# Kernel tuning notes

Hardware: AMD Instinct MI355X
Metric: run time of the kernel (lower is better)

The kernel has to match this reference:

```python
import jax, jax.numpy as jnp
import numpy as np
import math

HID = 1024
NH = 16
DH = HID // NH
B, S = 2, 2048

def _rel_shift(x):
    # x: [i, j, b, n] -> Transformer-XL relative shift
    i, j, b, n = x.shape
    xp = jnp.pad(x, ((0, 0), (1, 0), (0, 0), (0, 0)))  # [i, j+1, b, n]
    xp = xp.reshape(j + 1, i, b, n)
    return xp[1:].reshape(i, j, b, n)

def setup_inputs() -> dict:
    key = jax.random.key(0)
    ks = jax.random.split(key, 10)
    sc = 1.0 / math.sqrt(HID)
    return {
        "hidden_states": jax.random.normal(ks[0], (B, S, HID), jnp.float32),
        "r": jax.random.normal(ks[1], (S, HID), jnp.float32),
        "r_w_bias": jax.random.normal(ks[2], (NH, DH), jnp.float32) * 0.02,
        "r_r_bias": jax.random.normal(ks[3], (NH, DH), jnp.float32) * 0.02,
        "Wq": jax.random.normal(ks[4], (HID, HID), jnp.float32) * sc,
        "bq": jnp.zeros((HID,), jnp.float32),
        "Wk": jax.random.normal(ks[5], (HID, HID), jnp.float32) * sc,
        "bk": jnp.zeros((HID,), jnp.float32),
        "Wv": jax.random.normal(ks[6], (HID, HID), jnp.float32) * sc,
        "bv": jnp.zeros((HID,), jnp.float32),
        "Wr": jax.random.normal(ks[7], (HID, HID), jnp.float32) * sc,
    }

def reference(hidden_states, r, r_w_bias, r_r_bias, Wq, bq, Wk, bk, Wv, bv, Wr):
    b, s, h = hidden_states.shape
    # projections (weights stored [in, out])
    q = (hidden_states @ Wq + bq).reshape(b, s, NH, DH).transpose(1, 0, 2, 3)  # [s,b,nh,d]
    k = (hidden_states @ Wk + bk).reshape(b, s, NH, DH).transpose(1, 0, 2, 3)  # [s,b,nh,d]
    v = (hidden_states @ Wv + bv).reshape(b, s, NH, DH).transpose(0, 2, 1, 3)  # [b,nh,s,d]
    r_head_k = (r @ Wr).reshape(s, NH, DH)  # [rlen,nh,d]
    # content (AC) and position (BD) terms
    AC = jnp.einsum('ibnd,jbnd->ijbn', q + r_w_bias, k)
    BD = _rel_shift(jnp.einsum('ibnd,jnd->ijbn', q + r_r_bias, r_head_k))
    scores = (AC + BD).transpose(2, 3, 0, 1) / math.sqrt(DH)  # [b,nh,q,k]
    probs = jax.nn.softmax(scores, axis=-1)
    ctx = jnp.matmul(probs, v)  # [b,nh,q,d]
    ctx = ctx.transpose(0, 2, 1, 3).reshape(b, s, h)
    return ctx
```

## Files before the change

### kernel.cpp

```cpp
#include <hip/hip_runtime.h>
#include <math.h>

#define HID   1024
#define NHEAD 16
#define DHEAD 64
#define BATCH 2
#define SEQ   2048

#define TQ   64
#define TK2  128
#define NW2  191
#define LDP  136
#define LDBT 68

#define KSPLIT 2048
#define HEADSZ ((size_t)BATCH * SEQ * HID)

typedef __bf16 bf16_t;
typedef bf16_t bf16x8 __attribute__((ext_vector_type(8)));
typedef bf16_t bf16x4 __attribute__((ext_vector_type(4)));
typedef float  f32x4  __attribute__((ext_vector_type(4)));

__device__ __forceinline__ void load_lds16(const void* g, void* l) {
    __builtin_amdgcn_global_load_lds(
        (const __attribute__((address_space(1))) unsigned int*)g,
        (__attribute__((address_space(3))) unsigned int*)l, 16, 0, 0);
}

__device__ __forceinline__ void wg_barrier() {
    asm volatile("s_waitcnt lgkmcnt(0)" ::: "memory");
    __builtin_amdgcn_s_barrier();
    asm volatile("" ::: "memory");
}

__device__ __forceinline__ void split2(float x, bf16_t* hi, bf16_t* lo) {
    bf16_t h = (bf16_t)x;
    *hi = h;
    *lo = (bf16_t)(x - (float)h);
}

__global__ __launch_bounds__(256) void split_interleave(
    const float* __restrict__ in, bf16_t* __restrict__ out, int n4)
{
    int g = blockIdx.x * 256 + threadIdx.x;
    if (g >= n4) return;
    float4 v = ((const float4*)in)[g];
    int m = g >> 8, c4 = g & 255;
    float xs[4] = {v.x, v.y, v.z, v.w};
    bf16x8 o;
#pragma unroll
    for (int e = 0; e < 4; e++) {
        bf16_t h, l; split2(xs[e], &h, &l);
        o[2 * e] = h; o[2 * e + 1] = l;
    }
    *(bf16x8*)(out + (size_t)m * KSPLIT + c4 * 8) = o;
}

__global__ __launch_bounds__(256) void transpose_split3(
    const float* __restrict__ W0, const float* __restrict__ W1,
    const float* __restrict__ W2, bf16_t* __restrict__ WtBase)
{
    __shared__ float t[64][65];
    const int z = blockIdx.z;
    const float* W = (z == 0) ? W0 : (z == 1) ? W1 : W2;
    bf16_t* Wt = WtBase + (size_t)z * 1024 * KSPLIT;
    const int tid = threadIdx.x;
    const int n0 = blockIdx.x * 64, k0 = blockIdx.y * 64;
    for (int idx = tid; idx < 1024; idx += 256) {
        int r = idx >> 4, c4 = (idx & 15) * 4;
        float4 v = *(const float4*)(W + (size_t)(k0 + r) * HID + n0 + c4);
        t[r][c4] = v.x; t[r][c4 + 1] = v.y; t[r][c4 + 2] = v.z; t[r][c4 + 3] = v.w;
    }
    __syncthreads();
    for (int idx = tid; idx < 1024; idx += 256) {
        int nr = idx >> 4, c4 = (idx & 15) * 4;
        bf16x8 o;
#pragma unroll
        for (int e = 0; e < 4; e++) {
            bf16_t h, l; split2(t[c4 + e][nr], &h, &l);
            o[2 * e] = h; o[2 * e + 1] = l;
        }
        *(bf16x8*)(Wt + (size_t)(n0 + nr) * KSPLIT + (k0 + c4) * 2) = o;
    }
}

__global__ __launch_bounds__(256) void transpose_split(
    const float* __restrict__ W, bf16_t* __restrict__ Wt)
{
    __shared__ float t[64][65];
    const int tid = threadIdx.x;
    const int n0 = blockIdx.x * 64, k0 = blockIdx.y * 64;
    for (int idx = tid; idx < 1024; idx += 256) {
        int r = idx >> 4, c4 = (idx & 15) * 4;
        float4 v = *(const float4*)(W + (size_t)(k0 + r) * HID + n0 + c4);
        t[r][c4] = v.x; t[r][c4 + 1] = v.y; t[r][c4 + 2] = v.z; t[r][c4 + 3] = v.w;
    }
    __syncthreads();
    for (int idx = tid; idx < 1024; idx += 256) {
        int nr = idx >> 4, c4 = (idx & 15) * 4;
        bf16x8 o;
#pragma unroll
        for (int e = 0; e < 4; e++) {
            bf16_t h, l; split2(t[c4 + e][nr], &h, &l);
            o[2 * e] = h; o[2 * e + 1] = l;
        }
        *(bf16x8*)(Wt + (size_t)(n0 + nr) * KSPLIT + (k0 + c4) * 2) = o;
    }
}

__global__ __launch_bounds__(256, 3) void gemm_qkv_fused(
    const bf16_t* __restrict__ A, const bf16_t* __restrict__ Wt3,
    const float* __restrict__ bq, const float* __restrict__ bk,
    const float* __restrict__ bv, const float* __restrict__ rrb,
    bf16_t* __restrict__ Cq)
{
    __shared__ bf16_t As[128 * 64];
    __shared__ bf16_t Bs[128 * 64];
    const int tid = threadIdx.x;
    const int w = tid >> 6, lane = tid & 63;
    const int quad = lane >> 4, l16 = lane & 15;
    const int bn = blockIdx.x * 128;
    const int bm = blockIdx.y * 128;
    const int proj = bn >> 10;
    const int vswap = (proj == 2);

    const int srow = tid >> 3;
    const int scg  = (tid & 7) ^ ((tid >> 3) & 7);
    const bf16_t* Ab = A   + (size_t)(bm + srow) * KSPLIT + scg * 8;
    const bf16_t* Bb = Wt3 + (size_t)(bn + srow) * KSPLIT + scg * 8;

    f32x4 acc[2][8];
#pragma unroll
    for (int i = 0; i < 2; i++)
#pragma unroll
        for (int j = 0; j < 8; j++) {
            acc[i][j][0] = 0.f; acc[i][j][1] = 0.f;
            acc[i][j][2] = 0.f; acc[i][j][3] = 0.f;
        }

    const bf16_t* P1 = vswap ? Bs : As;
    const bf16_t* P2 = vswap ? As : Bs;

    for (int k0 = 0; k0 < KSPLIT; k0 += 64) {
#pragma unroll
        for (int j = 0; j < 4; j++) {
            load_lds16(Ab + (size_t)j * 32 * KSPLIT + k0, &As[j * 2048 + w * 512]);
            load_lds16(Bb + (size_t)j * 32 * KSPLIT + k0, &Bs[j * 2048 + w * 512]);
        }
        __syncthreads();
        bf16x8 af[2][2];
#pragma unroll
        for (int mt = 0; mt < 2; mt++) {
            int r = w * 32 + mt * 16 + l16, rx = r & 7;
            int c0 = (quad ^ rx);
            af[mt][0] = *(const bf16x8*)&P1[r * 64 + c0 * 8];
            af[mt][1] = *(const bf16x8*)&P1[r * 64 + (c0 ^ 4) * 8];
        }
#pragma unroll
        for (int nt = 0; nt < 8; nt++) {
            int r = nt * 16 + l16, rx = r & 7;
            int c0 = (quad ^ rx);
            bf16x8 b0 = *(const bf16x8*)&P2[r * 64 + c0 * 8];
            bf16x8 b1 = *(const bf16x8*)&P2[r * 64 + (c0 ^ 4) * 8];
#pragma unroll
            for (int mt = 0; mt < 2; mt++) {
                acc[mt][nt] = __builtin_amdgcn_mfma_f32_16x16x32_bf16(af[mt][0], b0, acc[mt][nt], 0, 0, 0);
                acc[mt][nt] = __builtin_amdgcn_mfma_f32_16x16x32_bf16(af[mt][1], b1, acc[mt][nt], 0, 0, 0);
            }
        }
        __syncthreads();
    }

#pragma unroll
    for (int mt = 0; mt < 2; mt++)
#pragma unroll
        for (int nt = 0; nt < 8; nt++)
#pragma unroll
            for (int r4 = 0; r4 < 4; r4++) {
                int rowp = w * 32 + mt * 16 + quad * 4 + r4;
                int colp = nt * 16 + l16;
                float v = acc[mt][nt][r4];
                if (!vswap) {
                    int m = bm + rowp, nloc = (bn & 1023) + colp;
                    v += (proj == 0) ? (bq[nloc] + rrb[nloc]) : bk[nloc];
                    int bb = m >> 11, s = m & (SEQ - 1);
                    int nh = nloc >> 6, d = nloc & 63;
                    Cq[(size_t)proj * HEADSZ + (((size_t)(bb * NHEAD + nh) * SEQ + s) * DHEAD) + d] = (bf16_t)v;
                } else {
                    int nloc = (bn & 1023) + rowp, m = bm + colp;
                    v += bv[nloc];
                    int bb = m >> 11, s = m & (SEQ - 1);
                    int nh = nloc >> 6, d = nloc & 63;
                    int j = s & 127;
                    int s2 = (s & ~127) | (((j & 15) << 3) | (j >> 4));
                    Cq[(size_t)2 * HEADSZ + (((size_t)(bb * NHEAD + nh) * DHEAD + d) * SEQ) + s2] = (bf16_t)v;
                }
            }
}

__global__ __launch_bounds__(256, 3) void gemm_split_mfma(
    const bf16_t* __restrict__ A, const bf16_t* __restrict__ Bw,
    bf16_t* __restrict__ C)
{
    __shared__ bf16_t As[128 * 64];
    __shared__ bf16_t Bs[128 * 64];
    const int tid = threadIdx.x;
    const int w = tid >> 6, lane = tid & 63;
    const int quad = lane >> 4, l16 = lane & 15;
    const int bn = blockIdx.x * 128;
    const int bm = blockIdx.y * 128;
    const int srow = tid >> 3;
    const int scg  = (tid & 7) ^ ((tid >> 3) & 7);
    const bf16_t* Ab = A  + (size_t)(bm + srow) * KSPLIT + scg * 8;
    const bf16_t* Bb = Bw + (size_t)(bn + srow) * KSPLIT + scg * 8;

    f32x4 acc[2][8];
#pragma unroll
    for (int i = 0; i < 2; i++)
#pragma unroll
        for (int j = 0; j < 8; j++) {
            acc[i][j][0] = 0.f; acc[i][j][1] = 0.f;
            acc[i][j][2] = 0.f; acc[i][j][3] = 0.f;
        }

    for (int k0 = 0; k0 < KSPLIT; k0 += 64) {
#pragma unroll
        for (int j = 0; j < 4; j++) {
            load_lds16(Ab + (size_t)j * 32 * KSPLIT + k0, &As[j * 2048 + w * 512]);
            load_lds16(Bb + (size_t)j * 32 * KSPLIT + k0, &Bs[j * 2048 + w * 512]);
        }
        __syncthreads();
        bf16x8 af[2][2];
#pragma unroll
        for (int mt = 0; mt < 2; mt++) {
            int r = w * 32 + mt * 16 + l16, rx = r & 7;
            int c0 = (quad ^ rx);
            af[mt][0] = *(const bf16x8*)&As[r * 64 + c0 * 8];
            af[mt][1] = *(const bf16x8*)&As[r * 64 + (c0 ^ 4) * 8];
        }
#pragma unroll
        for (int nt = 0; nt < 8; nt++) {
            int r = nt * 16 + l16, rx = r & 7;
            int c0 = (quad ^ rx);
            bf16x8 b0 = *(const bf16x8*)&Bs[r * 64 + c0 * 8];
            bf16x8 b1 = *(const bf16x8*)&Bs[r * 64 + (c0 ^ 4) * 8];
#pragma unroll
            for (int mt = 0; mt < 2; mt++) {
                acc[mt][nt] = __builtin_amdgcn_mfma_f32_16x16x32_bf16(af[mt][0], b0, acc[mt][nt], 0, 0, 0);
                acc[mt][nt] = __builtin_amdgcn_mfma_f32_16x16x32_bf16(af[mt][1], b1, acc[mt][nt], 0, 0, 0);
            }
        }
        __syncthreads();
    }
#pragma unroll
    for (int mt = 0; mt < 2; mt++)
#pragma unroll
        for (int nt = 0; nt < 8; nt++)
#pragma unroll
            for (int r4 = 0; r4 < 4; r4++) {
                int rowp = w * 32 + mt * 16 + quad * 4 + r4;
                int colp = nt * 16 + l16;
                int s = bm + rowp, n = bn + colp;
                int nh = n >> 6, d = n & 63;
                C[(((size_t)nh * SEQ + s) * DHEAD) + d] = (bf16_t)acc[mt][nt][r4];
            }
}

__global__ __launch_bounds__(256) void dcorr_kernel(
    const bf16_t* __restrict__ Kh, const float* __restrict__ rwb,
    const float* __restrict__ rrb, float* __restrict__ dc)
{
    int g = blockIdx.x * 256 + threadIdx.x;
    int bn = g >> 11;
    int n = bn & (NHEAD - 1);
    const bf16_t* kr = Kh + (size_t)g * DHEAD;
    float a = 0.f;
#pragma unroll
    for (int c8 = 0; c8 < 8; c8++) {
        bf16x8 kv = *(const bf16x8*)(kr + c8 * 8);
#pragma unroll
        for (int e = 0; e < 8; e++) {
            int d = c8 * 8 + e;
            a = fmaf(rwb[n * DHEAD + d] - rrb[n * DHEAD + d], (float)kv[e], a);
        }
    }
    dc[g] = a;
}

__global__ __launch_bounds__(256, 2) void rel_attn_mfma13(
    const bf16_t* __restrict__ Qh, const bf16_t* __restrict__ Kh,
    const bf16_t* __restrict__ Vth, const bf16_t* __restrict__ Rkh,
    const float* __restrict__ dcorr, const bf16_t* __restrict__ zp,
    float* __restrict__ Out)
{
    __shared__ bf16_t qs[65 * 64];
    __shared__ bf16_t ktP[64 * LDP];
    __shared__ bf16_t vt[64 * 128];
    __shared__ bf16_t rkb[192 * LDBT];
    __shared__ float dco[TK2];

    const int tid = threadIdx.x;
    const int w = tid >> 6, lane = tid & 63;
    const int quad = lane >> 4, l16 = lane & 15;

    const int L = blockIdx.x + (SEQ / TQ) * (blockIdx.y + NHEAD * blockIdx.z);
    const int xcd = L & 7, kk = L >> 3;
    const int nb = xcd * 4 + (kk >> 5);
    const int i0 = (kk & 31) * TQ;
    const int n = nb & (NHEAD - 1), b = nb >> 4;

    const bf16_t* Qb = Qh + ((size_t)(b * NHEAD + n) * SEQ + i0) * DHEAD;
    const bf16_t* Kb = Kh + (size_t)(b * NHEAD + n) * SEQ * DHEAD;
    const bf16_t* Vb = Vth + (size_t)(b * NHEAD + n) * DHEAD * SEQ;
    const bf16_t* Rb = Rkh + (size_t)n * SEQ * DHEAD;
    const float*  Db = dcorr + (size_t)(b * NHEAD + n) * SEQ;

    for (int idx = tid; idx < 65 * 8; idx += 256) {
        int row = idx >> 3, p = idx & 7;
        int g = p ^ (row & 7);
        uint4 val = make_uint4(0, 0, 0, 0);
        if (i0 + row < SEQ) val = *(const uint4*)(Qb + row * DHEAD + g * 8);
        *(uint4*)&qs[row * 64 + p * 8] = val;
    }
    __syncthreads();

    const int rq = 16 * w + l16;
    const int cq0 = quad ^ (rq & 7);
    const bf16x8 aq0 = *(const bf16x8*)&qs[rq * 64 + cq0 * 8];
    const bf16x8 aq1 = *(const bf16x8*)&qs[rq * 64 + (cq0 ^ 4) * 8];

    f32x4 o[4];
    float lsum[4];
#pragma unroll
    for (int t = 0; t < 4; t++) {
        o[t][0] = 0.f; o[t][1] = 0.f; o[t][2] = 0.f; o[t][3] = 0.f;
        lsum[t] = 0.f;
    }
    const float C1 = 0.18033688f;

    const int ltB = (3 - w) * 16;

    for (int j0 = 0; j0 < SEQ; j0 += TK2) {
        const int lstar = 64 + i0 - j0;
        const bool mixed = (lstar > 0) && (lstar < NW2);
        const bool needB4 = (lstar < NW2);
        const bool needBd64 = (lstar < 127);

        __syncthreads();
#pragma unroll
        for (int t = 0; t < 4; t++) {
            int r0 = (w + 4 * t) * 8;
            int row = r0 + (lane >> 3);
            int gch = (lane & 7) ^ (row & 7);
            load_lds16(Kb + (size_t)(j0 + row) * DHEAD + gch * 8, &ktP[r0 * 64]);
        }
        const int base1 = SEQ + j0 - i0 - TQ;
#pragma unroll
        for (int t = 0; t < 6; t++) {
            int l0 = (w + 4 * t) * 8;
            int l = l0 + (lane >> 3);
            int rr = base1 + l;
            const bf16_t* rp = (rr < SEQ) ? (Rb + (size_t)rr * DHEAD)
                             : (rr > SEQ) ? (Rb + (size_t)(rr - SEQ - 1) * DHEAD) : zp;
            int gch = (lane & 7) ^ (l & 7);
            load_lds16(rp + gch * 8, &rkb[l0 * 64]);
        }
        if (tid < 32) load_lds16(Db + j0 + tid * 4, dco);
#pragma unroll
        for (int t = 0; t < 4; t++) {
            int d0 = (w + 4 * t) * 4;
            int d = d0 + (lane >> 4);
            int gch = (lane & 15) ^ (d & 15);
            load_lds16(Vb + (size_t)d * SEQ + j0 + gch * 8, &vt[d0 * 128]);
        }
        asm volatile("s_waitcnt vmcnt(4)" ::: "memory");
        __builtin_amdgcn_s_barrier();
        asm volatile("" ::: "memory");

        f32x4 sac[8];
#pragma unroll
        for (int nt = 0; nt < 8; nt++) {
            int r = nt * 16 + l16;
            int c0 = quad ^ (r & 7);
            bf16x8 b0 = *(const bf16x8*)&ktP[r * 64 + c0 * 8];
            bf16x8 b1 = *(const bf16x8*)&ktP[r * 64 + (c0 ^ 4) * 8];
            f32x4 c; c[0] = 0.f; c[1] = 0.f; c[2] = 0.f; c[3] = 0.f;
            c = __builtin_amdgcn_mfma_f32_16x16x32_bf16(aq0, b0, c, 0, 0, 0);
            c = __builtin_amdgcn_mfma_f32_16x16x32_bf16(aq1, b1, c, 0, 0, 0);
            sac[nt] = c;
        }
        f32x4 bdc9[9];
#pragma unroll
        for (int lt8 = 0; lt8 < 9; lt8++) {
            int l = ltB + lt8 * 16 + l16;
            int c0 = quad ^ (l & 7);
            bf16x8 b0 = *(const bf16x8*)&rkb[l * 64 + c0 * 8];
            bf16x8 b1 = *(const bf16x8*)&rkb[l * 64 + (c0 ^ 4) * 8];
            f32x4 c; c[0] = 0.f; c[1] = 0.f; c[2] = 0.f; c[3] = 0.f;
            c = __builtin_amdgcn_mfma_f32_16x16x32_bf16(aq0, b0, c, 0, 0, 0);
            c = __builtin_amdgcn_mfma_f32_16x16x32_bf16(aq1, b1, c, 0, 0, 0);
            bdc9[lt8] = c;
        }
        float bd64 = 0.f;
        if (needBd64 && w >= 2) {
            int l = (w - 2) * 64 + lane;
            int lx = l & 7;
#pragma unroll
            for (int c = 0; c < 8; c++) {
                bf16x8 qv = *(const bf16x8*)&qs[64 * 64 + c * 8];
                bf16x8 rv = *(const bf16x8*)&rkb[l * 64 + (c ^ lx) * 8];
#pragma unroll
                for (int e = 0; e < 8; e++) bd64 = fmaf((float)qv[e], (float)rv[e], bd64);
            }
        }
        wg_barrier();

#pragma unroll
        for (int lt8 = 0; lt8 < 9; lt8++) {
            int l = ltB + lt8 * 16 + l16;
            bf16x4 pk;
#pragma unroll
            for (int r = 0; r < 4; r++) pk[r] = (bf16_t)bdc9[lt8][r];
            *(bf16x4*)&rkb[l * LDBT + 16 * w + quad * 4] = pk;
        }
        if (needBd64 && w >= 2) rkb[((w - 2) * 64 + lane) * LDBT + 64] = (bf16_t)bd64;
        if (needB4) wg_barrier();

        float sv[8][4];
        if (mixed) {
#pragma unroll
            for (int nt = 0; nt < 8; nt++) {
                float dcv = dco[nt * 16 + l16];
#pragma unroll
                for (int r = 0; r < 4; r++) {
                    int il = 16 * w + quad * 4 + r;
                    int jl = nt * 16 + l16;
                    int l = jl + (TQ - 1) - il;
                    int rr = base1 + l;
                    int ip = il + (rr > SEQ ? 1 : 0);
                    float bd = (float)rkb[l * LDBT + ip];
                    sv[nt][r] = sac[nt][r] + dcv + bd;
                }
            }
        } else {
            const int shift = (lstar <= 0) ? 1 : 0;
            const int il0 = 16 * w + quad * 4;
            const int base = (l16 + (TQ - 1) - il0) * LDBT + il0 + shift;
#pragma unroll
            for (int nt = 0; nt < 8; nt++) {
                float dcv = dco[nt * 16 + l16];
#pragma unroll
                for (int r = 0; r < 4; r++) {
                    float bd = (float)rkb[base + nt * 16 * LDBT - r * (LDBT - 1)];
                    sv[nt][r] = sac[nt][r] + dcv + bd;
                }
            }
        }

#pragma unroll
        for (int r = 0; r < 4; r++) {
            float s = 0.f;
#pragma unroll
            for (int nt = 0; nt < 8; nt++) {
                sv[nt][r] = exp2f(sv[nt][r] * C1);
                s += sv[nt][r];
            }
            lsum[r] += s;
        }

#pragma unroll
        for (int r = 0; r < 4; r++) {
            bf16x8 px;
#pragma unroll
            for (int nt = 0; nt < 8; nt++) px[nt] = (bf16_t)sv[nt][r];
            *(bf16x8*)&ktP[(16 * w + quad * 4 + r) * LDP + l16 * 8] = px;
        }

        bf16x8 pa[4];
#pragma unroll
        for (int c = 0; c < 4; c++)
            pa[c] = *(const bf16x8*)&ktP[(16 * w + l16) * LDP + c * 32 + quad * 8];
        asm volatile("s_waitcnt vmcnt(0)" ::: "memory");
        wg_barrier();
#pragma unroll
        for (int nt = 0; nt < 4; nt++) {
#pragma unroll
            for (int c = 0; c < 4; c++) {
                int dv = nt * 16 + l16;
                int gch = (4 * c + quad) ^ (dv & 15);
                bf16x8 vb = *(const bf16x8*)&vt[dv * 128 + gch * 8];
                o[nt] = __builtin_amdgcn_mfma_f32_16x16x32_bf16(pa[c], vb, o[nt], 0, 0, 0);
            }
        }
    }

    float inv[4];
#pragma unroll
    for (int r = 0; r < 4; r++) {
        float s = lsum[r];
        s += __shfl_xor(s, 1); s += __shfl_xor(s, 2);
        s += __shfl_xor(s, 4); s += __shfl_xor(s, 8);
        inv[r] = 1.f / s;
    }
#pragma unroll
    for (int nt = 0; nt < 4; nt++)
#pragma unroll
        for (int r = 0; r < 4; r++) {
            int gi = i0 + 16 * w + quad * 4 + r;
            Out[(size_t)(b * SEQ + gi) * HID + n * DHEAD + nt * 16 + l16] = o[nt][r] * inv[r];
        }
}

extern "C" void kernel_launch(void* const* d_in, const int* in_sizes, int n_in,
                              void* d_out, int out_size, void* d_ws, size_t ws_size,
                              hipStream_t stream) {
    const float* hs  = (const float*)d_in[0];
    const float* r   = (const float*)d_in[1];
    const float* rwb = (const float*)d_in[2];
    const float* rrb = (const float*)d_in[3];
    const float* Wq  = (const float*)d_in[4];
    const float* bq  = (const float*)d_in[5];
    const float* Wk  = (const float*)d_in[6];
    const float* bk  = (const float*)d_in[7];
    const float* Wv  = (const float*)d_in[8];
    const float* bv  = (const float*)d_in[9];
    const float* Wr  = (const float*)d_in[10];

    bf16_t* ws0 = (bf16_t*)d_ws;
    bf16_t* hsS = ws0;
    bf16_t* Wt3 = ws0 + (size_t)4096 * KSPLIT;
    bf16_t* Qh  = Wt3 + (size_t)3072 * KSPLIT;
    bf16_t* Kh  = Qh + HEADSZ;
    bf16_t* Vh  = Kh + HEADSZ;
    bf16_t* Rh  = Vh + HEADSZ;
    bf16_t* rS  = ws0;
    bf16_t* WtR = ws0 + (size_t)2048 * KSPLIT;
    float*  dcG = (float*)(ws0 + (size_t)3072 * KSPLIT);
    bf16_t* zp  = ws0 + (size_t)3072 * KSPLIT + 2 * BATCH * NHEAD * SEQ;

    dim3 blk(256);

    split_interleave<<<4096, blk, 0, stream>>>(hs, hsS, (BATCH * SEQ * HID) / 4);
    transpose_split3<<<dim3(16, 16, 3), blk, 0, stream>>>(Wq, Wk, Wv, Wt3);
    gemm_qkv_fused<<<dim3(24, 32), blk, 0, stream>>>(hsS, Wt3, bq, bk, bv, rrb, Qh);

    split_interleave<<<2048, blk, 0, stream>>>(r, rS, (SEQ * HID) / 4);
    transpose_split<<<dim3(16, 16), blk, 0, stream>>>(Wr, WtR);
    gemm_split_mfma<<<dim3(8, 16), blk, 0, stream>>>(rS, WtR, Rh);

    dcorr_kernel<<<(BATCH * NHEAD * SEQ) / 256, blk, 0, stream>>>(Kh, rwb, rrb, dcG);
    hipMemsetAsync(zp, 0, 256, stream);

    rel_attn_mfma13<<<dim3(SEQ / TQ, NHEAD, BATCH), blk, 0, stream>>>(
        Qh, Kh, Vh, Rh, dcG, zp, (float*)d_out);
}
```

Measured before the change: 356.0 us.

## Merge r-split, Wr transpose, dcorr and zero-pad into one launch; merge attention barriers

Four small preprocessing steps (split of r, transpose-split of Wr, the key-bias correction dot products, and the memset of the zero pad) now run as block-index ranges of a single kernel launch. This removes several launch gaps. In the attention kernel, the conditional barrier after writing the BD tile and the later barrier before the PV MFMA are merged into one unconditional barrier that also waits on outstanding global and LDS traffic. The merge cuts one barrier per key tile, but non-mixed tiles now always hit a barrier.

```diff
diff --git a/kernel.cpp b/kernel.cpp
--- a/kernel.cpp
+++ b/kernel.cpp
@@ -64,30 +64,6 @@
     const int z = blockIdx.z;
     const float* W = (z == 0) ? W0 : (z == 1) ? W1 : W2;
     bf16_t* Wt = WtBase + (size_t)z * 1024 * KSPLIT;
-    const int tid = threadIdx.x;
-    const int n0 = blockIdx.x * 64, k0 = blockIdx.y * 64;
-    for (int idx = tid; idx < 1024; idx += 256) {
-        int r = idx >> 4, c4 = (idx & 15) * 4;
-        float4 v = *(const float4*)(W + (size_t)(k0 + r) * HID + n0 + c4);
-        t[r][c4] = v.x; t[r][c4 + 1] = v.y; t[r][c4 + 2] = v.z; t[r][c4 + 3] = v.w;
-    }
-    __syncthreads();
-    for (int idx = tid; idx < 1024; idx += 256) {
-        int nr = idx >> 4, c4 = (idx & 15) * 4;
-        bf16x8 o;
-#pragma unroll
-        for (int e = 0; e < 4; e++) {
-            bf16_t h, l; split2(t[c4 + e][nr], &h, &l);
-            o[2 * e] = h; o[2 * e + 1] = l;
-        }
-        *(bf16x8*)(Wt + (size_t)(n0 + nr) * KSPLIT + (k0 + c4) * 2) = o;
-    }
-}
-
-__global__ __launch_bounds__(256) void transpose_split(
-    const float* __restrict__ W, bf16_t* __restrict__ Wt)
-{
-    __shared__ float t[64][65];
     const int tid = threadIdx.x;
     const int n0 = blockIdx.x * 64, k0 = blockIdx.y * 64;
     for (int idx = tid; idx < 1024; idx += 256) {
@@ -266,28 +242,68 @@
             }
 }
 
-__global__ __launch_bounds__(256) void dcorr_kernel(
+__global__ __launch_bounds__(256) void post_qkv_combo(
+    const float* __restrict__ r, bf16_t* __restrict__ rS,
+    const float* __restrict__ Wr, bf16_t* __restrict__ WtR,
     const bf16_t* __restrict__ Kh, const float* __restrict__ rwb,
-    const float* __restrict__ rrb, float* __restrict__ dc)
+    const float* __restrict__ rrb, float* __restrict__ dc,
+    bf16_t* __restrict__ zp)
 {
-    int g = blockIdx.x * 256 + threadIdx.x;
-    int bn = g >> 11;
-    int n = bn & (NHEAD - 1);
-    const bf16_t* kr = Kh + (size_t)g * DHEAD;
-    float a = 0.f;
-#pragma unroll
-    for (int c8 = 0; c8 < 8; c8++) {
-        bf16x8 kv = *(const bf16x8*)(kr + c8 * 8);
-#pragma unroll
-        for (int e = 0; e < 8; e++) {
-            int d = c8 * 8 + e;
-            a = fmaf(rwb[n * DHEAD + d] - rrb[n * DHEAD + d], (float)kv[e], a);
-        }
-    }
-    dc[g] = a;
-}
-
-__global__ __launch_bounds__(256, 2) void rel_attn_mfma13(
+    __shared__ float t[64][65];
+    const int bid = blockIdx.x;
+    const int tid = threadIdx.x;
+    if (bid < 2048) {
+        int g = bid * 256 + tid;
+        float4 v = ((const float4*)r)[g];
+        int m = g >> 8, c4 = g & 255;
+        float xs[4] = {v.x, v.y, v.z, v.w};
+        bf16x8 o;
+#pragma unroll
+        for (int e = 0; e < 4; e++) {
+            bf16_t h, l; split2(xs[e], &h, &l);
+            o[2 * e] = h; o[2 * e + 1] = l;
+        }
+        *(bf16x8*)(rS + (size_t)m * KSPLIT + c4 * 8) = o;
+    } else if (bid < 2304) {
+        int bb = bid - 2048;
+        const int n0 = (bb & 15) * 64, k0 = (bb >> 4) * 64;
+        for (int idx = tid; idx < 1024; idx += 256) {
+            int rr = idx >> 4, c4 = (idx & 15) * 4;
+            float4 v = *(const float4*)(Wr + (size_t)(k0 + rr) * HID + n0 + c4);
+            t[rr][c4] = v.x; t[rr][c4 + 1] = v.y; t[rr][c4 + 2] = v.z; t[rr][c4 + 3] = v.w;
+        }
+        __syncthreads();
+        for (int idx = tid; idx < 1024; idx += 256) {
+            int nr = idx >> 4, c4 = (idx & 15) * 4;
+            bf16x8 o;
+#pragma unroll
+            for (int e = 0; e < 4; e++) {
+                bf16_t h, l; split2(t[c4 + e][nr], &h, &l);
+                o[2 * e] = h; o[2 * e + 1] = l;
+            }
+            *(bf16x8*)(WtR + (size_t)(n0 + nr) * KSPLIT + (k0 + c4) * 2) = o;
+        }
+    } else {
+        int g = (bid - 2304) * 256 + tid;
+        int bn = g >> 11;
+        int n = bn & (NHEAD - 1);
+        const bf16_t* kr = Kh + (size_t)g * DHEAD;
+        float a = 0.f;
+#pragma unroll
+        for (int c8 = 0; c8 < 8; c8++) {
+            bf16x8 kv = *(const bf16x8*)(kr + c8 * 8);
+#pragma unroll
+            for (int e = 0; e < 8; e++) {
+                int d = c8 * 8 + e;
+                a = fmaf(rwb[n * DHEAD + d] - rrb[n * DHEAD + d], (float)kv[e], a);
+            }
+        }
+        dc[g] = a;
+        if (bid == 2304 && tid < 128) zp[tid] = (bf16_t)0.f;
+    }
+}
+
+__global__ __launch_bounds__(256, 2) void rel_attn_mfma14(
     const bf16_t* __restrict__ Qh, const bf16_t* __restrict__ Kh,
     const bf16_t* __restrict__ Vth, const bf16_t* __restrict__ Rkh,
     const float* __restrict__ dcorr, const bf16_t* __restrict__ zp,
@@ -343,7 +359,6 @@
     for (int j0 = 0; j0 < SEQ; j0 += TK2) {
         const int lstar = 64 + i0 - j0;
         const bool mixed = (lstar > 0) && (lstar < NW2);
-        const bool needB4 = (lstar < NW2);
         const bool needBd64 = (lstar < 127);
 
         __syncthreads();
@@ -424,7 +439,11 @@
             *(bf16x4*)&rkb[l * LDBT + 16 * w + quad * 4] = pk;
         }
         if (needBd64 && w >= 2) rkb[((w - 2) * 64 + lane) * LDBT + 64] = (bf16_t)bd64;
-        if (needB4) wg_barrier();
+
+        asm volatile("s_waitcnt vmcnt(0)" ::: "memory");
+        asm volatile("s_waitcnt lgkmcnt(0)" ::: "memory");
+        __builtin_amdgcn_s_barrier();
+        asm volatile("" ::: "memory");
 
         float sv[8][4];
         if (mixed) {
@@ -480,8 +499,6 @@
 #pragma unroll
         for (int c = 0; c < 4; c++)
             pa[c] = *(const bf16x8*)&ktP[(16 * w + l16) * LDP + c * 32 + quad * 8];
-        asm volatile("s_waitcnt vmcnt(0)" ::: "memory");
-        wg_barrier();
 #pragma unroll
         for (int nt = 0; nt < 4; nt++) {
 #pragma unroll
@@ -544,13 +561,10 @@
     transpose_split3<<<dim3(16, 16, 3), blk, 0, stream>>>(Wq, Wk, Wv, Wt3);
     gemm_qkv_fused<<<dim3(24, 32), blk, 0, stream>>>(hsS, Wt3, bq, bk, bv, rrb, Qh);
 
-    split_interleave<<<2048, blk, 0, stream>>>(r, rS, (SEQ * HID) / 4);
-    transpose_split<<<dim3(16, 16), blk, 0, stream>>>(Wr, WtR);
+    post_qkv_combo<<<2560, blk, 0, stream>>>(r, rS, Wr, WtR, Kh, rwb, rrb, dcG, zp);
+
     gemm_split_mfma<<<dim3(8, 16), blk, 0, stream>>>(rS, WtR, Rh);
 
-    dcorr_kernel<<<(BATCH * NHEAD * SEQ) / 256, blk, 0, stream>>>(Kh, rwb, rrb, dcG);
-    hipMemsetAsync(zp, 0, 256, stream);
-
-    rel_attn_mfma13<<<dim3(SEQ / TQ, NHEAD, BATCH), blk, 0, stream>>>(
+    rel_attn_mfma14<<<dim3(SEQ / TQ, NHEAD, BATCH), blk, 0, stream>>>(
         Qh, Kh, Vh, Rh, dcG, zp, (float*)d_out);
 }
```

Result: faster. 346.4 us (-2.7%).
